# Performance work log

Measured on AMD Instinct MI355X. Metric: run time of the kernel, lower is better.

Reference implementation:

```python
import jax, jax.numpy as jnp
import numpy as np

N = 100000      # nodes
DEG = 16        # avg degree
E = N * DEG     # edges
D = 128         # feature dim
U = 128         # output units


def setup_inputs() -> dict:
    key = jax.random.key(0)
    k1, k2, k3, k4 = jax.random.split(key, 4)
    node_features = jax.random.normal(k1, (N, D), dtype=jnp.float32)
    # every row has exactly DEG entries so the 'mean' combiner never divides by zero
    edge_rows = jnp.arange(E, dtype=jnp.int64) // DEG
    edge_cols = jax.random.randint(k2, (E,), 0, N, dtype=jnp.int64)
    edge_weights = jax.random.uniform(k3, (E,), dtype=jnp.float32, minval=0.1, maxval=1.0)
    W = jax.random.normal(k4, (D, U), dtype=jnp.float32) * (1.0 / np.sqrt(D))
    b = jnp.zeros((U,), dtype=jnp.float32)
    return {"node_features": node_features, "edge_rows": edge_rows,
            "edge_cols": edge_cols, "edge_weights": edge_weights, "W": W, "b": b}


def reference(node_features, edge_rows, edge_cols, edge_weights, W, b):
    # embedding_lookup_sparse_v2 with combiner='mean':
    # agg[i] = sum_j w_ij * feat[j] / sum_j w_ij
    gathered = node_features[edge_cols] * edge_weights[:, None]   # [E, D]
    num = jax.ops.segment_sum(gathered, edge_rows, num_segments=N)  # [N, D]
    den = jax.ops.segment_sum(edge_weights, edge_rows, num_segments=N)  # [N]
    agg = num / den[:, None]
    # Dense(units, activation='relu'); dropout/l2_norm are built but not applied in call()
    return jax.nn.relu(agg @ W + b)
```

## Files before the change

### kernel.cpp

```cpp
#include <hip/hip_runtime.h>

#define N_NODES 100000
#define DEG 16
#define D_DIM 128
#define U_DIM 128

typedef __bf16 bf16x8 __attribute__((ext_vector_type(8)));
typedef float f32x4 __attribute__((ext_vector_type(4)));

__device__ __forceinline__ unsigned short f2bf(float x) {
    unsigned int u = __float_as_uint(x);
    u += 0x7fffu + ((u >> 16) & 1u);
    return (unsigned short)(u >> 16);
}
__device__ __forceinline__ unsigned int pack2(float a, float b) {
    return (unsigned int)f2bf(a) | ((unsigned int)f2bf(b) << 16);
}

__global__ __launch_bounds__(256)
void ymat_kernel(const float* __restrict__ feat,
                 const float* __restrict__ W,
                 const float* __restrict__ bias,
                 unsigned short* __restrict__ Y) {
    const int lane = threadIdx.x & 63;
    const int wv = threadIdx.x >> 6;
    const int quad = lane >> 4;
    const int l15 = lane & 15;
    const int n0 = blockIdx.x * 128;
    const int u_base = wv * 32;

    bf16x8 afr[2][4];
    #pragma unroll
    for (int ni = 0; ni < 2; ++ni) {
        const int u = u_base + ni * 16 + l15;
        #pragma unroll
        for (int kc = 0; kc < 4; ++kc) {
            union { unsigned short us[8]; bf16x8 v; } pk;
            #pragma unroll
            for (int j = 0; j < 8; ++j)
                pk.us[j] = f2bf(W[(kc * 32 + quad * 8 + j) * 128 + u]);
            afr[ni][kc] = pk.v;
        }
    }
    float4 bv0 = *(const float4*)(bias + u_base + quad * 4);
    float4 bv1 = *(const float4*)(bias + u_base + 16 + quad * 4);

    for (int mi = 0; mi < 8; ++mi) {
        const int node = n0 + mi * 16 + l15;
        const int rowc = node < N_NODES ? node : N_NODES - 1;
        bf16x8 bfr[4];
        #pragma unroll
        for (int kc = 0; kc < 4; ++kc) {
            const float* ap = feat + (size_t)rowc * D_DIM + kc * 32 + quad * 8;
            const float4 a0 = *(const float4*)ap;
            const float4 a1 = *(const float4*)(ap + 4);
            union { unsigned short us[8]; bf16x8 v; } pk;
            pk.us[0] = f2bf(a0.x); pk.us[1] = f2bf(a0.y);
            pk.us[2] = f2bf(a0.z); pk.us[3] = f2bf(a0.w);
            pk.us[4] = f2bf(a1.x); pk.us[5] = f2bf(a1.y);
            pk.us[6] = f2bf(a1.z); pk.us[7] = f2bf(a1.w);
            bfr[kc] = pk.v;
        }
        f32x4 acc0 = (f32x4){0.f, 0.f, 0.f, 0.f};
        f32x4 acc1 = (f32x4){0.f, 0.f, 0.f, 0.f};
        #pragma unroll
        for (int kc = 0; kc < 4; ++kc) {
            acc0 = __builtin_amdgcn_mfma_f32_16x16x32_bf16(afr[0][kc], bfr[kc], acc0, 0, 0, 0);
            acc1 = __builtin_amdgcn_mfma_f32_16x16x32_bf16(afr[1][kc], bfr[kc], acc1, 0, 0, 0);
        }
        if (node < N_NODES) {
            unsigned int* yp = (unsigned int*)(Y + (size_t)node * U_DIM + u_base + quad * 4);
            uint2 s0, s1;
            s0.x = pack2(acc0[0] + bv0.x, acc0[1] + bv0.y);
            s0.y = pack2(acc0[2] + bv0.z, acc0[3] + bv0.w);
            s1.x = pack2(acc1[0] + bv1.x, acc1[1] + bv1.y);
            s1.y = pack2(acc1[2] + bv1.z, acc1[3] + bv1.w);
            *(uint2*)yp = s0;
            *(uint2*)(yp + 8) = s1;
        }
    }
}

__global__ __launch_bounds__(256, 4)
void agg_kernel(const unsigned short* __restrict__ Y,
                const int* __restrict__ cols,
                const float* __restrict__ wts,
                float* __restrict__ out) {
    const int node = blockIdx.x * 16 + (threadIdx.x >> 4);
    const int d = threadIdx.x & 15;
    const int e0 = node * DEG;

    int cc[DEG];
    float ww[DEG];
    #pragma unroll
    for (int q = 0; q < 4; ++q) {
        const int4 c4 = *(const int4*)(cols + e0 + 4 * q);
        const float4 w4 = *(const float4*)(wts + e0 + 4 * q);
        cc[4 * q + 0] = c4.x; cc[4 * q + 1] = c4.y;
        cc[4 * q + 2] = c4.z; cc[4 * q + 3] = c4.w;
        ww[4 * q + 0] = w4.x; ww[4 * q + 1] = w4.y;
        ww[4 * q + 2] = w4.z; ww[4 * q + 3] = w4.w;
    }
    float den = 0.f;
    #pragma unroll
    for (int e = 0; e < DEG; ++e) den += ww[e];

    float a0 = 0.f, a1 = 0.f, a2 = 0.f, a3 = 0.f;
    float a4 = 0.f, a5 = 0.f, a6 = 0.f, a7 = 0.f;
    #pragma unroll
    for (int h = 0; h < 2; ++h) {
        uint4 p[8];
        #pragma unroll
        for (int e = 0; e < 8; ++e)
            p[e] = *(const uint4*)(Y + (size_t)cc[h * 8 + e] * U_DIM + d * 8);
        #pragma unroll
        for (int e = 0; e < 8; ++e) {
            const float w = ww[h * 8 + e];
            a0 = fmaf(w, __uint_as_float(p[e].x << 16), a0);
            a1 = fmaf(w, __uint_as_float(p[e].x & 0xffff0000u), a1);
            a2 = fmaf(w, __uint_as_float(p[e].y << 16), a2);
            a3 = fmaf(w, __uint_as_float(p[e].y & 0xffff0000u), a3);
            a4 = fmaf(w, __uint_as_float(p[e].z << 16), a4);
            a5 = fmaf(w, __uint_as_float(p[e].z & 0xffff0000u), a5);
            a6 = fmaf(w, __uint_as_float(p[e].w << 16), a6);
            a7 = fmaf(w, __uint_as_float(p[e].w & 0xffff0000u), a7);
        }
    }
    const float inv = 1.0f / den;
    f32x4 o0, o1;
    o0[0] = fmaxf(a0 * inv, 0.f); o0[1] = fmaxf(a1 * inv, 0.f);
    o0[2] = fmaxf(a2 * inv, 0.f); o0[3] = fmaxf(a3 * inv, 0.f);
    o1[0] = fmaxf(a4 * inv, 0.f); o1[1] = fmaxf(a5 * inv, 0.f);
    o1[2] = fmaxf(a6 * inv, 0.f); o1[3] = fmaxf(a7 * inv, 0.f);
    f32x4* op = (f32x4*)(out + (size_t)node * U_DIM + d * 8);
    __builtin_nontemporal_store(o0, op);
    __builtin_nontemporal_store(o1, op + 1);
}

extern "C" void kernel_launch(void* const* d_in, const int* in_sizes, int n_in,
                              void* d_out, int out_size, void* d_ws, size_t ws_size,
                              hipStream_t stream) {
    const float* feat = (const float*)d_in[0];
    const int* cols  = (const int*)d_in[2];
    const float* wts = (const float*)d_in[3];
    const float* W   = (const float*)d_in[4];
    const float* b   = (const float*)d_in[5];
    float* out = (float*)d_out;

    unsigned short* Y = (unsigned short*)d_ws;

    const int nblocks = (N_NODES + 127) / 128;
    ymat_kernel<<<nblocks, 256, 0, stream>>>(feat, W, b, Y);

    agg_kernel<<<N_NODES / 16, 256, 0, stream>>>(Y, cols, wts, out);
}
```

Before: 196.0 us.

## Pre-cast W to transposed bf16 and split aggregation into two column-half phases

Adds a small kernel that converts W to bf16 in transposed layout, so each ymat block loads its MFMA A-fragments with one vector load instead of 32 strided fp32 loads plus conversions. The aggregation kernel is restructured so each block handles 32 nodes but only 64 of the 128 output columns, with the first 3125 blocks covering the low half and the rest the high half. The aim is a smaller gathered working set of Y per phase, for better L2 hit rates on the random neighbor gathers. The cost is an extra kernel launch and reading cols and weights twice.

```diff
diff --git a/kernel.cpp b/kernel.cpp
--- a/kernel.cpp
+++ b/kernel.cpp
@@ -17,9 +17,16 @@
     return (unsigned int)f2bf(a) | ((unsigned int)f2bf(b) << 16);
 }
 
+__global__ void cast_w_kernel(const float* __restrict__ W,
+                              unsigned short* __restrict__ WT) {
+    int t = blockIdx.x * 256 + threadIdx.x;
+    int k = t >> 7, n = t & 127;
+    WT[n * 128 + k] = f2bf(W[t]);
+}
+
 __global__ __launch_bounds__(256)
 void ymat_kernel(const float* __restrict__ feat,
-                 const float* __restrict__ W,
+                 const unsigned short* __restrict__ WT,
                  const float* __restrict__ bias,
                  unsigned short* __restrict__ Y) {
     const int lane = threadIdx.x & 63;
@@ -34,13 +41,8 @@
     for (int ni = 0; ni < 2; ++ni) {
         const int u = u_base + ni * 16 + l15;
         #pragma unroll
-        for (int kc = 0; kc < 4; ++kc) {
-            union { unsigned short us[8]; bf16x8 v; } pk;
-            #pragma unroll
-            for (int j = 0; j < 8; ++j)
-                pk.us[j] = f2bf(W[(kc * 32 + quad * 8 + j) * 128 + u]);
-            afr[ni][kc] = pk.v;
-        }
+        for (int kc = 0; kc < 4; ++kc)
+            afr[ni][kc] = *(const bf16x8*)(WT + u * 128 + kc * 32 + quad * 8);
     }
     float4 bv0 = *(const float4*)(bias + u_base + quad * 4);
     float4 bv1 = *(const float4*)(bias + u_base + 16 + quad * 4);
@@ -86,8 +88,10 @@
                 const int* __restrict__ cols,
                 const float* __restrict__ wts,
                 float* __restrict__ out) {
-    const int node = blockIdx.x * 16 + (threadIdx.x >> 4);
-    const int d = threadIdx.x & 15;
+    const int phase = (blockIdx.x >= 3125) ? 1 : 0;
+    const int nb = blockIdx.x - phase * 3125;
+    const int node = nb * 32 + (threadIdx.x >> 3);
+    const int ubase = phase * 64 + (threadIdx.x & 7) * 8;
     const int e0 = node * DEG;
 
     int cc[DEG];
@@ -112,7 +116,7 @@
         uint4 p[8];
         #pragma unroll
         for (int e = 0; e < 8; ++e)
-            p[e] = *(const uint4*)(Y + (size_t)cc[h * 8 + e] * U_DIM + d * 8);
+            p[e] = *(const uint4*)(Y + (size_t)cc[h * 8 + e] * U_DIM + ubase);
         #pragma unroll
         for (int e = 0; e < 8; ++e) {
             const float w = ww[h * 8 + e];
@@ -132,7 +136,7 @@
     o0[2] = fmaxf(a2 * inv, 0.f); o0[3] = fmaxf(a3 * inv, 0.f);
     o1[0] = fmaxf(a4 * inv, 0.f); o1[1] = fmaxf(a5 * inv, 0.f);
     o1[2] = fmaxf(a6 * inv, 0.f); o1[3] = fmaxf(a7 * inv, 0.f);
-    f32x4* op = (f32x4*)(out + (size_t)node * U_DIM + d * 8);
+    f32x4* op = (f32x4*)(out + (size_t)node * U_DIM + ubase);
     __builtin_nontemporal_store(o0, op);
     __builtin_nontemporal_store(o1, op + 1);
 }
@@ -147,10 +151,13 @@
     const float* b   = (const float*)d_in[5];
     float* out = (float*)d_out;
 
-    unsigned short* Y = (unsigned short*)d_ws;
+    unsigned short* wt_bf = (unsigned short*)d_ws;
+    unsigned short* Y     = (unsigned short*)((char*)d_ws + 32768);
+
+    cast_w_kernel<<<16384 / 256, 256, 0, stream>>>(W, wt_bf);
 
     const int nblocks = (N_NODES + 127) / 128;
-    ymat_kernel<<<nblocks, 256, 0, stream>>>(feat, W, b, Y);
+    ymat_kernel<<<nblocks, 256, 0, stream>>>(feat, wt_bf, b, Y);
 
-    agg_kernel<<<N_NODES / 16, 256, 0, stream>>>(Y, cols, wts, out);
+    agg_kernel<<<6250, 256, 0, stream>>>(Y, cols, wts, out);
 }
```

Result: faster. 192.0 us (-2.0%).
